# Performance work log

Measured on AMD Instinct MI355X. Metric: run time of the kernel, lower is better.

## Reference

```python
import jax, jax.numpy as jnp
import numpy as np

N, E, B = 40000, 640000, 256
F_IN, H, D = 128, 128, 128  # num_node_features, hidden_dim, last_dim
EPS = 1e-5


def sage_conv(x, src, dst, Wl, bl, Wr, num_nodes):
    # PyG SAGEConv (mean aggr): out = lin_l(mean_j x_j) + lin_r(x)
    msg = x[src]                                            # [E, d] gather
    agg = jax.ops.segment_sum(msg, dst, num_segments=num_nodes)
    cnt = jax.ops.segment_sum(jnp.ones((src.shape[0],), x.dtype), dst,
                              num_segments=num_nodes)
    mean = agg / jnp.maximum(cnt, 1.0)[:, None]
    return mean @ Wl.T + bl + x @ Wr.T


def bn_eval(x, g, b, rm, rv):
    return g * (x - rm) * jax.lax.rsqrt(rv + EPS) + b


def lstm_cell(inp, h, c, Wih, Whh, bih, bhh):
    gates = inp @ Wih.T + h @ Whh.T + bih + bhh             # [B, 4D]
    i, f, g, o = jnp.split(gates, 4, axis=-1)
    c = jax.nn.sigmoid(f) * c + jax.nn.sigmoid(i) * jnp.tanh(g)
    h = jax.nn.sigmoid(o) * jnp.tanh(c)
    return h, c


def set2set(x, batch, Wih, Whh, bih, bhh, num_graphs, steps=3):
    d = x.shape[1]
    q_star = jnp.zeros((num_graphs, 2 * d), x.dtype)
    h = jnp.zeros((num_graphs, d), x.dtype)
    c = jnp.zeros((num_graphs, d), x.dtype)
    for _ in range(steps):
        h, c = lstm_cell(q_star, h, c, Wih, Whh, bih, bhh)
        q = h                                               # [B, D]
        e = jnp.sum(x * q[batch], axis=-1)                  # [N]
        emax = jax.ops.segment_max(e, batch, num_segments=num_graphs)
        a = jnp.exp(e - emax[batch])
        denom = jax.ops.segment_sum(a, batch, num_segments=num_graphs)
        a = a / denom[batch]
        r = jax.ops.segment_sum(a[:, None] * x, batch, num_segments=num_graphs)
        q_star = jnp.concatenate([q, r], axis=-1)
    return q_star


def setup_inputs() -> dict:
    key = jax.random.key(0)
    ks = jax.random.split(key, 20)
    x = jax.random.normal(ks[0], (N, F_IN), jnp.float32)
    edge_index = jax.random.randint(ks[1], (2, E), 0, N)
    batch = jnp.sort(jax.random.randint(ks[2], (N,), 0, B))
    s1, s2, sd = 1.0 / np.sqrt(F_IN), 1.0 / np.sqrt(H), 1.0 / np.sqrt(D)
    return {
        "x": x, "edge_index": edge_index, "batch": batch,
        "W1l": jax.random.normal(ks[3], (H, F_IN)) * s1,
        "b1l": jnp.zeros((H,)),
        "W1r": jax.random.normal(ks[4], (H, F_IN)) * s1,
        "g1": jnp.ones((H,)), "beta1": jnp.zeros((H,)),
        "rm1": jax.random.normal(ks[5], (H,)) * 0.1,
        "rv1": jax.random.uniform(ks[6], (H,), minval=0.5, maxval=1.5),
        "W2l": jax.random.normal(ks[7], (D, H)) * s2,
        "b2l": jnp.zeros((D,)),
        "W2r": jax.random.normal(ks[8], (D, H)) * s2,
        "g2": jnp.ones((D,)), "beta2": jnp.zeros((D,)),
        "rm2": jax.random.normal(ks[9], (D,)) * 0.1,
        "rv2": jax.random.uniform(ks[10], (D,), minval=0.5, maxval=1.5),
        "Wih": jax.random.normal(ks[11], (4 * D, 2 * D)) * sd,
        "Whh": jax.random.normal(ks[12], (4 * D, D)) * sd,
        "bih": jnp.zeros((4 * D,)), "bhh": jnp.zeros((4 * D,)),
        "Wp": jax.random.normal(ks[13], (D, 2 * D)) * sd,
        "bp": jnp.zeros((D,)),
    }


def reference(x, edge_index, batch, W1l, b1l, W1r, g1, beta1, rm1, rv1,
              W2l, b2l, W2r, g2, beta2, rm2, rv2, Wih, Whh, bih, bhh, Wp, bp):
    src, dst = edge_index[0], edge_index[1]
    num_nodes = x.shape[0]
    h1 = jax.nn.relu(bn_eval(sage_conv(x, src, dst, W1l, b1l, W1r, num_nodes),
                             g1, beta1, rm1, rv1))
    # dropout is identity in eval mode
    h2 = jax.nn.relu(bn_eval(sage_conv(h1, src, dst, W2l, b2l, W2r, num_nodes),
                             g2, beta2, rm2, rv2))
    q_star = set2set(h2, batch, Wih, Whh, bih, bhh, B, steps=3)  # [B, 2D]
    return q_star @ Wp.T + bp                                    # [B, D]
```

## Files before the change

### kernel.cpp

```cpp
#include <hip/hip_runtime.h>
#include <hip/hip_bf16.h>
#include <math.h>

#define NN 40000
#define NE 640000
#define NG 256
#define FD 128
#define SLOT 96

typedef __attribute__((ext_vector_type(8))) short bf16x8;
typedef __attribute__((ext_vector_type(4))) float f32x4;

__device__ __forceinline__ float sigf(float x) { return 1.f / (1.f + __expf(-x)); }
__device__ __forceinline__ unsigned short f2b(float f) {
    unsigned int u = __float_as_uint(f);
    return (unsigned short)((u + 0x7FFFu + ((u >> 16) & 1u)) >> 16);
}
__device__ __forceinline__ float b2f(unsigned int u16) {
    return __uint_as_float(u16 << 16);
}

__global__ void k_setup(const int* __restrict__ ei, const int* __restrict__ batch,
                        int* __restrict__ gptr, int* __restrict__ dcnt,
                        int* __restrict__ srcs,
                        const float* __restrict__ W1l, const float* __restrict__ W1r,
                        const float* __restrict__ W2l, const float* __restrict__ W2r,
                        unsigned short* __restrict__ Wb,
                        const float* __restrict__ Wihf, const float* __restrict__ Whhf,
                        unsigned short* __restrict__ Wb2) {
    int blk = blockIdx.x, t = threadIdx.x;
    if (blk < 625) {
        int i = blk * 256 + t;
        int4 s4 = ((const int4*)ei)[i];
        int4 d4 = ((const int4*)(ei + NE))[i];
        int p0 = atomicAdd(&dcnt[d4.x], 1);
        if (p0 < SLOT) srcs[d4.x * SLOT + p0] = s4.x;
        int p1 = atomicAdd(&dcnt[d4.y], 1);
        if (p1 < SLOT) srcs[d4.y * SLOT + p1] = s4.y;
        int p2 = atomicAdd(&dcnt[d4.z], 1);
        if (p2 < SLOT) srcs[d4.z * SLOT + p2] = s4.z;
        int p3 = atomicAdd(&dcnt[d4.w], 1);
        if (p3 < SLOT) srcs[d4.w * SLOT + p3] = s4.w;
    } else if (blk < 782) {
        int i = (blk - 625) * 256 + t;
        if (i >= NN) return;
        int b = batch[i];
        int pb = (i == 0) ? -1 : batch[i - 1];
        for (int g = pb + 1; g <= b; g++) gptr[g] = i;
        if (i == NN - 1)
            for (int g = b + 1; g <= NG; g++) gptr[g] = NN;
    } else if (blk < 846) {
        int j4 = (blk - 782) * 256 + t;
        int seg = j4 >> 12, off4 = j4 & 4095;
        const float* W = (seg == 0) ? W1l : (seg == 1) ? W1r : (seg == 2) ? W2l : W2r;
        float4 v = ((const float4*)W)[off4];
        ushort4 o;
        o.x = f2b(v.x); o.y = f2b(v.y); o.z = f2b(v.z); o.w = f2b(v.w);
        *(ushort4*)(Wb + (size_t)j4 * 4) = o;
    } else {
        int j4 = (blk - 846) * 256 + t;
        float4 v;
        size_t off;
        if (j4 < 32768) {
            int r = j4 >> 6, f4 = j4 & 63;
            int c = f4 >> 1, h = f4 & 1;
            v = ((const float4*)Wihf)[j4];
            off = ((size_t)c * 512 + r) * 8 + h * 4;
        } else {
            int jj = j4 - 32768;
            int r = jj >> 5, f4 = jj & 31;
            int c = f4 >> 1, h = f4 & 1;
            v = ((const float4*)Whhf)[jj];
            off = (size_t)512 * 256 + ((size_t)c * 512 + r) * 8 + h * 4;
        }
        ushort4 o;
        o.x = f2b(v.x); o.y = f2b(v.y); o.z = f2b(v.z); o.w = f2b(v.w);
        *(ushort4*)(Wb2 + off) = o;
    }
}

__global__ __launch_bounds__(256) void k_mm(
    const void* __restrict__ Av, int a_fp32,
    const unsigned short* __restrict__ W,
    unsigned short* __restrict__ C)
{
    __shared__ unsigned short Ws[128 * 128];
    int t = threadIdx.x;
    int nh = blockIdx.x & 1;
    int mblk = blockIdx.x >> 1;
    {
        const uint4* Wg = (const uint4*)(W + nh * 128 * 128);
#pragma unroll
        for (int i = 0; i < 8; i++) {
            int f = i * 256 + t;
            int row = f >> 4, c = f & 15;
            int cs = c ^ (row & 15);
            *(uint4*)&Ws[row * 128 + cs * 8] = Wg[f];
        }
    }
    __syncthreads();
    int w = t >> 6, lane = t & 63;
    int ln = lane & 15, quad = lane >> 4;
    int m0 = mblk * 64 + w * 16;
    bf16x8 a[4];
    if (a_fp32) {
        const float* Arow = (const float*)Av + (size_t)(m0 + ln) * 128;
#pragma unroll
        for (int ks = 0; ks < 4; ks++) {
            float4 u0 = *(const float4*)(Arow + ks * 32 + quad * 8);
            float4 u1 = *(const float4*)(Arow + ks * 32 + quad * 8 + 4);
            unsigned short tmp[8];
            tmp[0] = f2b(u0.x); tmp[1] = f2b(u0.y); tmp[2] = f2b(u0.z); tmp[3] = f2b(u0.w);
            tmp[4] = f2b(u1.x); tmp[5] = f2b(u1.y); tmp[6] = f2b(u1.z); tmp[7] = f2b(u1.w);
            a[ks] = *(const bf16x8*)tmp;
        }
    } else {
        const unsigned short* Arow = (const unsigned short*)Av + (size_t)(m0 + ln) * 128;
#pragma unroll
        for (int ks = 0; ks < 4; ks++)
            a[ks] = *(const bf16x8*)(Arow + ks * 32 + quad * 8);
    }
    for (int nt = 0; nt < 8; nt++) {
        int n0 = nt * 16;
        int row = n0 + ln;
        f32x4 acc = {0.f, 0.f, 0.f, 0.f};
#pragma unroll
        for (int ks = 0; ks < 4; ks++) {
            int c = ks * 4 + quad;
            bf16x8 b = *(const bf16x8*)&Ws[row * 128 + (c ^ (row & 15)) * 8];
            acc = __builtin_amdgcn_mfma_f32_16x16x32_bf16(a[ks], b, acc, 0, 0, 0);
        }
        size_t base = (size_t)(m0 + quad * 4) * 256 + nh * 128 + n0 + ln;
#pragma unroll
        for (int r = 0; r < 4; r++)
            C[base + (size_t)r * 256] = f2b(acc[r]);
    }
}

__global__ __launch_bounds__(256) void k_gather2(
    const unsigned short* __restrict__ C, const int* __restrict__ srcs,
    const int* __restrict__ dcnt,
    const float* __restrict__ bl,
    const float* __restrict__ gam, const float* __restrict__ bet,
    const float* __restrict__ rme, const float* __restrict__ rva,
    unsigned short* __restrict__ H)
{
    int t = threadIdx.x;
    int qw = t >> 4, l4 = t & 15;
    int node = blockIdx.x * 16 + qw;
    int deg = dcnt[node];
    int cnt = (deg < SLOT) ? deg : SLOT;
    int s0 = node * SLOT, e0 = s0 + cnt;
    const uint4* C4 = (const uint4*)C;
    float ac[8];
#pragma unroll
    for (int k = 0; k < 8; k++) ac[k] = 0.f;
    int i = s0;
    for (; i + 7 < e0; i += 8) {
        uint4 v0 = C4[(size_t)srcs[i]     * 32 + l4];
        uint4 v1 = C4[(size_t)srcs[i + 1] * 32 + l4];
        uint4 v2 = C4[(size_t)srcs[i + 2] * 32 + l4];
        uint4 v3 = C4[(size_t)srcs[i + 3] * 32 + l4];
        uint4 v4 = C4[(size_t)srcs[i + 4] * 32 + l4];
        uint4 v5 = C4[(size_t)srcs[i + 5] * 32 + l4];
        uint4 v6 = C4[(size_t)srcs[i + 6] * 32 + l4];
        uint4 v7 = C4[(size_t)srcs[i + 7] * 32 + l4];
        ac[0] += b2f(v0.x & 0xFFFFu) + b2f(v1.x & 0xFFFFu) + b2f(v2.x & 0xFFFFu) + b2f(v3.x & 0xFFFFu)
               + b2f(v4.x & 0xFFFFu) + b2f(v5.x & 0xFFFFu) + b2f(v6.x & 0xFFFFu) + b2f(v7.x & 0xFFFFu);
        ac[1] += b2f(v0.x >> 16) + b2f(v1.x >> 16) + b2f(v2.x >> 16) + b2f(v3.x >> 16)
               + b2f(v4.x >> 16) + b2f(v5.x >> 16) + b2f(v6.x >> 16) + b2f(v7.x >> 16);
        ac[2] += b2f(v0.y & 0xFFFFu) + b2f(v1.y & 0xFFFFu) + b2f(v2.y & 0xFFFFu) + b2f(v3.y & 0xFFFFu)
               + b2f(v4.y & 0xFFFFu) + b2f(v5.y & 0xFFFFu) + b2f(v6.y & 0xFFFFu) + b2f(v7.y & 0xFFFFu);
        ac[3] += b2f(v0.y >> 16) + b2f(v1.y >> 16) + b2f(v2.y >> 16) + b2f(v3.y >> 16)
               + b2f(v4.y >> 16) + b2f(v5.y >> 16) + b2f(v6.y >> 16) + b2f(v7.y >> 16);
        ac[4] += b2f(v0.z & 0xFFFFu) + b2f(v1.z & 0xFFFFu) + b2f(v2.z & 0xFFFFu) + b2f(v3.z & 0xFFFFu)
               + b2f(v4.z & 0xFFFFu) + b2f(v5.z & 0xFFFFu) + b2f(v6.z & 0xFFFFu) + b2f(v7.z & 0xFFFFu);
        ac[5] += b2f(v0.z >> 16) + b2f(v1.z >> 16) + b2f(v2.z >> 16) + b2f(v3.z >> 16)
               + b2f(v4.z >> 16) + b2f(v5.z >> 16) + b2f(v6.z >> 16) + b2f(v7.z >> 16);
        ac[6] += b2f(v0.w & 0xFFFFu) + b2f(v1.w & 0xFFFFu) + b2f(v2.w & 0xFFFFu) + b2f(v3.w & 0xFFFFu)
               + b2f(v4.w & 0xFFFFu) + b2f(v5.w & 0xFFFFu) + b2f(v6.w & 0xFFFFu) + b2f(v7.w & 0xFFFFu);
        ac[7] += b2f(v0.w >> 16) + b2f(v1.w >> 16) + b2f(v2.w >> 16) + b2f(v3.w >> 16)
               + b2f(v4.w >> 16) + b2f(v5.w >> 16) + b2f(v6.w >> 16) + b2f(v7.w >> 16);
    }
    for (; i < e0; i++) {
        uint4 v = C4[(size_t)srcs[i] * 32 + l4];
        ac[0] += b2f(v.x & 0xFFFFu); ac[1] += b2f(v.x >> 16);
        ac[2] += b2f(v.y & 0xFFFFu); ac[3] += b2f(v.y >> 16);
        ac[4] += b2f(v.z & 0xFFFFu); ac[5] += b2f(v.z >> 16);
        ac[6] += b2f(v.w & 0xFFFFu); ac[7] += b2f(v.w >> 16);
    }
    float inv = 1.0f / fmaxf((float)deg, 1.0f);
    uint4 yr = C4[(size_t)node * 32 + 16 + l4];
    float yo[8];
    yo[0] = b2f(yr.x & 0xFFFFu); yo[1] = b2f(yr.x >> 16);
    yo[2] = b2f(yr.y & 0xFFFFu); yo[3] = b2f(yr.y >> 16);
    yo[4] = b2f(yr.z & 0xFFFFu); yo[5] = b2f(yr.z >> 16);
    yo[6] = b2f(yr.w & 0xFFFFu); yo[7] = b2f(yr.w >> 16);
    float4 ga = ((const float4*)gam)[l4 * 2],     gb = ((const float4*)gam)[l4 * 2 + 1];
    float4 va = ((const float4*)rva)[l4 * 2],     vb = ((const float4*)rva)[l4 * 2 + 1];
    float4 ma = ((const float4*)rme)[l4 * 2],     mb = ((const float4*)rme)[l4 * 2 + 1];
    float4 ba = ((const float4*)bet)[l4 * 2],     bb = ((const float4*)bet)[l4 * 2 + 1];
    float4 la = ((const float4*)bl)[l4 * 2],      lb = ((const float4*)bl)[l4 * 2 + 1];
    float g[8] = {ga.x, ga.y, ga.z, ga.w, gb.x, gb.y, gb.z, gb.w};
    float rv[8] = {va.x, va.y, va.z, va.w, vb.x, vb.y, vb.z, vb.w};
    float rm[8] = {ma.x, ma.y, ma.z, ma.w, mb.x, mb.y, mb.z, mb.w};
    float bt[8] = {ba.x, ba.y, ba.z, ba.w, bb.x, bb.y, bb.z, bb.w};
    float lv[8] = {la.x, la.y, la.z, la.w, lb.x, lb.y, lb.z, lb.w};
    unsigned short o[8];
#pragma unroll
    for (int k = 0; k < 8; k++) {
        float y = ac[k] * inv + yo[k] + lv[k];
        float z = g[k] * rsqrtf(rv[k] + 1e-5f) * (y - rm[k]) + bt[k];
        o[k] = f2b(fmaxf(z, 0.f));
    }
    *(uint4*)(H + (size_t)node * 128 + l4 * 8) = *(const uint4*)o;
}

__global__ __launch_bounds__(512) void k_s2s(
    const unsigned short* __restrict__ h2, const int* __restrict__ gptr,
    const float* __restrict__ bih, const float* __restrict__ bhh,
    const unsigned short* __restrict__ Wihb, const unsigned short* __restrict__ Whhb,
    const float* __restrict__ Wp, const float* __restrict__ bp,
    float* __restrict__ out)
{
    int b = blockIdx.x, t = threadIdx.x;
    int wave = t >> 6, lane = t & 63;
    __shared__ float hs[FD];
    __shared__ float qstar[2 * FD];
    __shared__ float gates_s[512];
    __shared__ float wm[8], wd[8], red[8][FD];
    float creg = 0.f;
    int start = gptr[b], end = gptr[b + 1];
    const unsigned int* H2 = (const unsigned int*)h2;

    for (int step = 0; step < 3; step++) {
        if (step == 0) {
            if (t < FD) {
                float ig = bih[t] + bhh[t];
                float gg = bih[2 * FD + t] + bhh[2 * FD + t];
                float og = bih[3 * FD + t] + bhh[3 * FD + t];
                float c = sigf(ig) * tanhf(gg);
                float h = sigf(og) * tanhf(c);
                creg = c; hs[t] = h;
            }
        } else {
            float acc = bih[t] + bhh[t];
            const uint4* wi = (const uint4*)Wihb;
            for (int k = 0; k < 32; k++) {
                uint4 u = wi[k * 512 + t];
                const float* q = &qstar[k * 8];
                acc += b2f(u.x & 0xFFFFu)*q[0] + b2f(u.x >> 16)*q[1]
                     + b2f(u.y & 0xFFFFu)*q[2] + b2f(u.y >> 16)*q[3]
                     + b2f(u.z & 0xFFFFu)*q[4] + b2f(u.z >> 16)*q[5]
                     + b2f(u.w & 0xFFFFu)*q[6] + b2f(u.w >> 16)*q[7];
            }
            const uint4* wh = (const uint4*)Whhb;
            for (int k = 0; k < 16; k++) {
                uint4 u = wh[k * 512 + t];
                const float* hq = &hs[k * 8];
                acc += b2f(u.x & 0xFFFFu)*hq[0] + b2f(u.x >> 16)*hq[1]
                     + b2f(u.y & 0xFFFFu)*hq[2] + b2f(u.y >> 16)*hq[3]
                     + b2f(u.z & 0xFFFFu)*hq[4] + b2f(u.z >> 16)*hq[5]
                     + b2f(u.w & 0xFFFFu)*hq[6] + b2f(u.w >> 16)*hq[7];
            }
            gates_s[t] = acc;
            __syncthreads();
            if (t < FD) {
                float ig = gates_s[t], fg = gates_s[FD + t];
                float gg = gates_s[2 * FD + t], og = gates_s[3 * FD + t];
                float c = sigf(fg) * creg + sigf(ig) * tanhf(gg);
                float h = sigf(og) * tanhf(c);
                creg = c; hs[t] = h;
            }
        }
        __syncthreads();

        float2 q = ((const float2*)hs)[lane];
        float mw = -INFINITY, dw = 0.f, rx = 0.f, ry = 0.f;
        for (int n = start + wave; n < end; n += 8) {
            unsigned int u = H2[(size_t)n * 64 + lane];
            float vx = b2f(u & 0xFFFFu), vy = b2f(u >> 16);
            float e = vx * q.x + vy * q.y;
#pragma unroll
            for (int off = 32; off; off >>= 1) e += __shfl_xor(e, off);
            float mn = fmaxf(mw, e);
            float corr = __expf(mw - mn);
            float a = __expf(e - mn);
            rx = rx * corr + a * vx;
            ry = ry * corr + a * vy;
            dw = dw * corr + a;
            mw = mn;
        }
        if (lane == 0) wm[wave] = mw;
        __syncthreads();
        float M = wm[0];
#pragma unroll
        for (int k = 1; k < 8; k++) M = fmaxf(M, wm[k]);
        float cr = (M == -INFINITY) ? 0.f : __expf(mw - M);
        red[wave][2 * lane] = rx * cr;
        red[wave][2 * lane + 1] = ry * cr;
        if (lane == 0) wd[wave] = dw * cr;
        __syncthreads();
        if (t < FD) {
            float r = 0.f, den = 0.f;
#pragma unroll
            for (int k = 0; k < 8; k++) { r += red[k][t]; den += wd[k]; }
            float rn = (den > 0.f) ? r / den : 0.f;
            qstar[t] = hs[t];
            qstar[FD + t] = rn;
        }
        __syncthreads();
    }

    if (t < FD) {
        const float4* w4 = (const float4*)(Wp + (size_t)t * 256);
        const float4* q4 = (const float4*)qstar;
        float acc = bp[t];
        for (int k = 0; k < 64; k++) {
            float4 wv = w4[k], qv = q4[k];
            acc += qv.x*wv.x + qv.y*wv.y + qv.z*wv.z + qv.w*wv.w;
        }
        out[(size_t)b * FD + t] = acc;
    }
}

__global__ void k_zero_out(float* __restrict__ out, int n) {
    int i = blockIdx.x * blockDim.x + threadIdx.x;
    if (i < n) out[i] = 0.f;
}

extern "C" void kernel_launch(void* const* d_in, const int* in_sizes, int n_in,
                              void* d_out, int out_size, void* d_ws, size_t ws_size,
                              hipStream_t stream) {
    const float* x   = (const float*)d_in[0];
    const int*  ei    = (const int*)d_in[1];
    const int*  batch = (const int*)d_in[2];
    const float* W1l = (const float*)d_in[3];
    const float* b1l = (const float*)d_in[4];
    const float* W1r = (const float*)d_in[5];
    const float* g1  = (const float*)d_in[6];
    const float* be1 = (const float*)d_in[7];
    const float* rm1 = (const float*)d_in[8];
    const float* rv1 = (const float*)d_in[9];
    const float* W2l = (const float*)d_in[10];
    const float* b2l = (const float*)d_in[11];
    const float* W2r = (const float*)d_in[12];
    const float* g2  = (const float*)d_in[13];
    const float* be2 = (const float*)d_in[14];
    const float* rm2 = (const float*)d_in[15];
    const float* rv2 = (const float*)d_in[16];
    const float* Wih = (const float*)d_in[17];
    const float* Whh = (const float*)d_in[18];
    const float* bih = (const float*)d_in[19];
    const float* bhh = (const float*)d_in[20];
    const float* Wp  = (const float*)d_in[21];
    const float* bp  = (const float*)d_in[22];
    float* out = (float*)d_out;

    auto al = [](size_t s) { return (s + 255) & ~(size_t)255; };
    size_t off_dcnt = 0;
    size_t off_gptr = off_dcnt + al((size_t)NN * 4);
    size_t off_srcs = off_gptr + al((size_t)(NG + 1) * 4);
    size_t off_h2b  = off_srcs + al((size_t)NN * SLOT * 4);
    size_t off_h1b  = off_h2b  + al((size_t)NN * FD * 2);
    size_t off_Wb   = off_h1b  + al((size_t)NN * FD * 2);
    size_t off_Wb2  = off_Wb   + al((size_t)2 * 256 * 128 * 2);
    size_t off_C    = off_Wb2  + al((size_t)(512 * 256 + 512 * 128) * 2);
    size_t need     = off_C    + al((size_t)NN * 256 * 2);

    if (ws_size < need) {
        k_zero_out<<<(out_size + 255) / 256, 256, 0, stream>>>(out, out_size);
        return;
    }

    char* p = (char*)d_ws;
    int* dcnt    = (int*)(p + off_dcnt);
    int* gptr    = (int*)(p + off_gptr);
    int* srcs    = (int*)(p + off_srcs);
    unsigned short* h2b = (unsigned short*)(p + off_h2b);
    unsigned short* h1b = (unsigned short*)(p + off_h1b);
    unsigned short* Wb  = (unsigned short*)(p + off_Wb);
    unsigned short* Wb2 = (unsigned short*)(p + off_Wb2);
    unsigned short* C   = (unsigned short*)(p + off_C);

    hipMemsetAsync(dcnt, 0, (size_t)NN * 4, stream);

    k_setup<<<1038, 256, 0, stream>>>(ei, batch, gptr, dcnt, srcs,
                                      W1l, W1r, W2l, W2r, Wb, Wih, Whh, Wb2);

    k_mm<<<1250, 256, 0, stream>>>(x, 1, Wb, C);
    k_gather2<<<NN / 16, 256, 0, stream>>>(C, srcs, dcnt, b1l, g1, be1, rm1, rv1, h1b);

    k_mm<<<1250, 256, 0, stream>>>(h1b, 0, Wb + 32768, C);
    k_gather2<<<NN / 16, 256, 0, stream>>>(C, srcs, dcnt, b2l, g2, be2, rm2, rv2, h2b);

    k_s2s<<<NG, 512, 0, stream>>>(h2b, gptr, bih, bhh,
                                  Wb2, Wb2 + 512 * 256, Wp, bp, out);
}
```

Baseline: 264.5 us.

## Use 1024-thread set2set blocks with two-pass softmax for small graphs

Doubles the set2set block to 16 waves so each graph's node scan has twice the parallelism. For graphs of at most 512 nodes, it replaces the online rescaling softmax with two passes. Scores are cached in shared memory, then the node rows are re-read to accumulate exp-weighted sums without per-node correction exps. The cost is a second read of h2 rows, more shared memory, and larger blocks that may limit occupancy, though only 256 blocks are launched.

```diff
diff --git a/kernel.cpp b/kernel.cpp
--- a/kernel.cpp
+++ b/kernel.cpp
@@ -216,7 +216,7 @@
     *(uint4*)(H + (size_t)node * 128 + l4 * 8) = *(const uint4*)o;
 }
 
-__global__ __launch_bounds__(512) void k_s2s(
+__global__ __launch_bounds__(1024) void k_s2s(
     const unsigned short* __restrict__ h2, const int* __restrict__ gptr,
     const float* __restrict__ bih, const float* __restrict__ bhh,
     const unsigned short* __restrict__ Wihb, const unsigned short* __restrict__ Whhb,
@@ -228,9 +228,11 @@
     __shared__ float hs[FD];
     __shared__ float qstar[2 * FD];
     __shared__ float gates_s[512];
-    __shared__ float wm[8], wd[8], red[8][FD];
+    __shared__ float es[512];
+    __shared__ float wm[16], wd[16], red[16][FD];
     float creg = 0.f;
     int start = gptr[b], end = gptr[b + 1];
+    int seg = end - start;
     const unsigned int* H2 = (const unsigned int*)h2;
 
     for (int step = 0; step < 3; step++) {
@@ -244,26 +246,28 @@
                 creg = c; hs[t] = h;
             }
         } else {
-            float acc = bih[t] + bhh[t];
-            const uint4* wi = (const uint4*)Wihb;
-            for (int k = 0; k < 32; k++) {
-                uint4 u = wi[k * 512 + t];
-                const float* q = &qstar[k * 8];
-                acc += b2f(u.x & 0xFFFFu)*q[0] + b2f(u.x >> 16)*q[1]
-                     + b2f(u.y & 0xFFFFu)*q[2] + b2f(u.y >> 16)*q[3]
-                     + b2f(u.z & 0xFFFFu)*q[4] + b2f(u.z >> 16)*q[5]
-                     + b2f(u.w & 0xFFFFu)*q[6] + b2f(u.w >> 16)*q[7];
-            }
-            const uint4* wh = (const uint4*)Whhb;
-            for (int k = 0; k < 16; k++) {
-                uint4 u = wh[k * 512 + t];
-                const float* hq = &hs[k * 8];
-                acc += b2f(u.x & 0xFFFFu)*hq[0] + b2f(u.x >> 16)*hq[1]
-                     + b2f(u.y & 0xFFFFu)*hq[2] + b2f(u.y >> 16)*hq[3]
-                     + b2f(u.z & 0xFFFFu)*hq[4] + b2f(u.z >> 16)*hq[5]
-                     + b2f(u.w & 0xFFFFu)*hq[6] + b2f(u.w >> 16)*hq[7];
-            }
-            gates_s[t] = acc;
+            if (t < 512) {
+                float acc = bih[t] + bhh[t];
+                const uint4* wi = (const uint4*)Wihb;
+                for (int k = 0; k < 32; k++) {
+                    uint4 u = wi[k * 512 + t];
+                    const float* q = &qstar[k * 8];
+                    acc += b2f(u.x & 0xFFFFu)*q[0] + b2f(u.x >> 16)*q[1]
+                         + b2f(u.y & 0xFFFFu)*q[2] + b2f(u.y >> 16)*q[3]
+                         + b2f(u.z & 0xFFFFu)*q[4] + b2f(u.z >> 16)*q[5]
+                         + b2f(u.w & 0xFFFFu)*q[6] + b2f(u.w >> 16)*q[7];
+                }
+                const uint4* wh = (const uint4*)Whhb;
+                for (int k = 0; k < 16; k++) {
+                    uint4 u = wh[k * 512 + t];
+                    const float* hq = &hs[k * 8];
+                    acc += b2f(u.x & 0xFFFFu)*hq[0] + b2f(u.x >> 16)*hq[1]
+                         + b2f(u.y & 0xFFFFu)*hq[2] + b2f(u.y >> 16)*hq[3]
+                         + b2f(u.z & 0xFFFFu)*hq[4] + b2f(u.z >> 16)*hq[5]
+                         + b2f(u.w & 0xFFFFu)*hq[6] + b2f(u.w >> 16)*hq[7];
+                }
+                gates_s[t] = acc;
+            }
             __syncthreads();
             if (t < FD) {
                 float ig = gates_s[t], fg = gates_s[FD + t];
@@ -276,35 +280,64 @@
         __syncthreads();
 
         float2 q = ((const float2*)hs)[lane];
-        float mw = -INFINITY, dw = 0.f, rx = 0.f, ry = 0.f;
-        for (int n = start + wave; n < end; n += 8) {
-            unsigned int u = H2[(size_t)n * 64 + lane];
-            float vx = b2f(u & 0xFFFFu), vy = b2f(u >> 16);
-            float e = vx * q.x + vy * q.y;
-#pragma unroll
-            for (int off = 32; off; off >>= 1) e += __shfl_xor(e, off);
-            float mn = fmaxf(mw, e);
-            float corr = __expf(mw - mn);
-            float a = __expf(e - mn);
-            rx = rx * corr + a * vx;
-            ry = ry * corr + a * vy;
-            dw = dw * corr + a;
-            mw = mn;
-        }
-        if (lane == 0) wm[wave] = mw;
-        __syncthreads();
-        float M = wm[0];
-#pragma unroll
-        for (int k = 1; k < 8; k++) M = fmaxf(M, wm[k]);
-        float cr = (M == -INFINITY) ? 0.f : __expf(mw - M);
-        red[wave][2 * lane] = rx * cr;
-        red[wave][2 * lane + 1] = ry * cr;
-        if (lane == 0) wd[wave] = dw * cr;
+        float rx = 0.f, ry = 0.f, dw = 0.f;
+
+        if (seg <= 512) {
+            float mw = -INFINITY;
+            for (int n = start + wave; n < end; n += 16) {
+                unsigned int u = H2[(size_t)n * 64 + lane];
+                float vx = b2f(u & 0xFFFFu), vy = b2f(u >> 16);
+                float e = vx * q.x + vy * q.y;
+#pragma unroll
+                for (int off = 32; off; off >>= 1) e += __shfl_xor(e, off);
+                if (lane == 0) es[n - start] = e;
+                mw = fmaxf(mw, e);
+            }
+            if (lane == 0) wm[wave] = mw;
+            __syncthreads();
+            float M = wm[0];
+#pragma unroll
+            for (int k = 1; k < 16; k++) M = fmaxf(M, wm[k]);
+            for (int n = start + wave; n < end; n += 16) {
+                unsigned int u = H2[(size_t)n * 64 + lane];
+                float vx = b2f(u & 0xFFFFu), vy = b2f(u >> 16);
+                float a = __expf(es[n - start] - M);
+                rx += a * vx; ry += a * vy; dw += a;
+            }
+            red[wave][2 * lane] = rx;
+            red[wave][2 * lane + 1] = ry;
+            if (lane == 0) wd[wave] = dw;
+        } else {
+            float mw = -INFINITY;
+            for (int n = start + wave; n < end; n += 16) {
+                unsigned int u = H2[(size_t)n * 64 + lane];
+                float vx = b2f(u & 0xFFFFu), vy = b2f(u >> 16);
+                float e = vx * q.x + vy * q.y;
+#pragma unroll
+                for (int off = 32; off; off >>= 1) e += __shfl_xor(e, off);
+                float mn = fmaxf(mw, e);
+                float corr = __expf(mw - mn);
+                float a = __expf(e - mn);
+                rx = rx * corr + a * vx;
+                ry = ry * corr + a * vy;
+                dw = dw * corr + a;
+                mw = mn;
+            }
+            if (lane == 0) wm[wave] = mw;
+            __syncthreads();
+            float M = wm[0];
+#pragma unroll
+            for (int k = 1; k < 16; k++) M = fmaxf(M, wm[k]);
+            float cr = (M == -INFINITY) ? 0.f : __expf(mw - M);
+            red[wave][2 * lane] = rx * cr;
+            red[wave][2 * lane + 1] = ry * cr;
+            if (lane == 0) wd[wave] = dw * cr;
+        }
         __syncthreads();
         if (t < FD) {
             float r = 0.f, den = 0.f;
 #pragma unroll
-            for (int k = 0; k < 8; k++) { r += red[k][t]; den += wd[k]; }
+            for (int k = 0; k < 16; k++) { r += red[k][t]; den += wd[k]; }
             float rn = (den > 0.f) ? r / den : 0.f;
             qstar[t] = hs[t];
             qstar[FD + t] = rn;
@@ -394,6 +427,6 @@
     k_mm<<<1250, 256, 0, stream>>>(h1b, 0, Wb + 32768, C);
     k_gather2<<<NN / 16, 256, 0, stream>>>(C, srcs, dcnt, b2l, g2, be2, rm2, rv2, h2b);
 
-    k_s2s<<<NG, 512, 0, stream>>>(h2b, gptr, bih, bhh,
-                                  Wb2, Wb2 + 512 * 256, Wp, bp, out);
-}
+    k_s2s<<<NG, 1024, 0, stream>>>(h2b, gptr, bih, bhh,
+                                   Wb2, Wb2 + 512 * 256, Wp, bp, out);
+}
```

After: 259.8 us. About the same (-1.8%).
